# Kernel tuning notes

Hardware: AMD Instinct MI355X
Metric: run time of the kernel (lower is better)

The kernel has to match this reference:

```python
import math
import jax, jax.numpy as jnp
import numpy as np

B_, H_, L_, N_ = 64, 256, 1024, 64  # batch, n_feat, n_embd(=seq len), complex state modes (d_state=128 -> 64 conj pairs)


def setup_inputs() -> dict:
    key = jax.random.key(0)
    ks = jax.random.split(key, 12)
    x = jax.random.normal(ks[0], (B_, H_, L_), jnp.float32)
    t = jax.random.randint(ks[1], (B_,), 0, 1000)
    # AdaLayerNorm linear: n_embd -> 2*n_embd
    ada_w = jax.random.normal(ks[2], (2 * L_, L_), jnp.float32) * 0.02
    ada_b = jnp.zeros((2 * L_,), jnp.float32)
    # S4Layer prenorm (LayerNorm over n_feat, affine)
    norm_w = jnp.ones((H_,), jnp.float32)
    norm_b = jnp.zeros((H_,), jnp.float32)
    # S4D-style diagonal SSM parameters
    log_dt = math.log(0.001) + jax.random.uniform(ks[3], (H_,), jnp.float32) * (math.log(0.1) - math.log(0.001))
    A_re = jnp.full((H_, N_), math.log(0.5), jnp.float32)            # A_real = -exp(A_re) = -0.5
    A_im = jnp.ones((H_, 1), jnp.float32) * (math.pi * jnp.arange(N_, dtype=jnp.float32))[None, :]
    C_re = jax.random.normal(ks[4], (2, H_, N_), jnp.float32) * (N_ ** -0.5)  # 2 channels: bidirectional
    C_im = jax.random.normal(ks[5], (2, H_, N_), jnp.float32) * (N_ ** -0.5)
    D = jax.random.normal(ks[6], (H_,), jnp.float32)
    out_w = jax.random.normal(ks[7], (H_, H_), jnp.float32) * (H_ ** -0.5)   # S4 output 1x1 conv
    out_b = jnp.zeros((H_,), jnp.float32)
    lin1_w = jax.random.normal(ks[8], (H_, H_), jnp.float32) * (H_ ** -0.5)
    lin1_b = jnp.zeros((H_,), jnp.float32)
    lin2_w = jax.random.normal(ks[9], (H_, H_), jnp.float32) * (H_ ** -0.5)
    lin2_b = jnp.zeros((H_,), jnp.float32)
    return dict(x=x, t=t, ada_w=ada_w, ada_b=ada_b, norm_w=norm_w, norm_b=norm_b,
                log_dt=log_dt, A_re=A_re, A_im=A_im, C_re=C_re, C_im=C_im, D=D,
                out_w=out_w, out_b=out_b, lin1_w=lin1_w, lin1_b=lin1_b,
                lin2_w=lin2_w, lin2_b=lin2_b)


def _ln(v):
    m = v.mean(-1, keepdims=True)
    s = v.var(-1, keepdims=True)
    return (v - m) * jax.lax.rsqrt(s + 1e-5)


def _forward(t, x, ada_w, ada_b, norm_w, norm_b, log_dt, A_re, A_im, C_re, C_im, D,
             out_w, out_b, lin1_w, lin1_b, lin2_w, lin2_b):
    B, H, L = x.shape
    # ---- AdaLayerNorm over last dim (n_embd = L) ----
    half = L // 2
    freqs = jnp.exp(jnp.arange(half, dtype=jnp.float32) * (-math.log(10000.0) / (half - 1)))
    emb = t.astype(jnp.float32)[:, None] * freqs[None, :]
    emb = jnp.concatenate([jnp.sin(emb), jnp.cos(emb)], axis=-1)           # (B, L)
    emb = jax.nn.silu(emb) @ ada_w.T + ada_b                                # (B, 2L)
    scale, shift = jnp.split(emb[:, None, :], 2, axis=2)                    # (B,1,L)
    x = _ln(x) * (1.0 + scale) + shift                                      # (B,H,L)
    # ---- S4Layer: prenorm over channels ----
    z = (_ln(x.transpose(0, 2, 1)) * norm_w + norm_b).transpose(0, 2, 1)    # (B,H,L)
    # ---- S4 (diagonal SSM) bidirectional FFT convolution ----
    dt = jnp.exp(log_dt)                                                    # (H,)
    A = -jnp.exp(A_re) + 1j * A_im                                          # (H,N)
    dtA = dt[:, None] * A
    dA = jnp.exp(dtA)
    C = (C_re + 1j * C_im) * ((dA - 1.0) / A)                               # ZOH-discretized (2,H,N)
    vand = jnp.exp(dtA[:, :, None] * jnp.arange(L, dtype=jnp.float32))      # (H,N,L)
    K = 2.0 * jnp.real(jnp.einsum('chn,hnl->chl', C, vand))                 # (2,H,L)
    k = jnp.pad(K[0], ((0, 0), (0, L))) + jnp.pad(K[1][:, ::-1], ((0, 0), (L, 0)))  # (H,2L)
    n = 2 * L
    y = jnp.fft.irfft(jnp.fft.rfft(z, n=n) * jnp.fft.rfft(k, n=n), n=n)[..., :L]
    y = y + D[:, None] * z
    y = jax.nn.gelu(y, approximate=False)
    y = jnp.einsum('oi,bil->bol', out_w, y) + out_b[None, :, None]          # S4 output 1x1 conv
    x2 = y + x                                                              # residual
    # ---- gated output ----
    g = jnp.tanh(x2) * jax.nn.sigmoid(x2)
    out1 = jnp.einsum('oi,bil->bol', lin1_w, g) + lin1_b[None, :, None] + x
    out2 = jnp.einsum('oi,bil->bol', lin2_w, g) + lin2_b[None, :, None]
    return (out1, out2)


def reference(x, t, ada_w, ada_b, norm_w, norm_b, log_dt, A_re, A_im, C_re, C_im, D,
              out_w, out_b, lin1_w, lin1_b, lin2_w, lin2_b):
    return _forward(t, x, ada_w, ada_b, norm_w, norm_b, log_dt, A_re, A_im, C_re, C_im,
                    D, out_w, out_b, lin1_w, lin1_b, lin2_w, lin2_b)
```

## Files before the change

### kernel.cpp

```cpp
#include <hip/hip_runtime.h>
#include <math.h>

#define Bq 64
#define Hq 256
#define Lq 1024
#define HLq (Hq*Lq)
#define BHLq (Bq*Hq*Lq)
#define HNq (Hq*64)

typedef __attribute__((ext_vector_type(8))) short bf16x8;
typedef __attribute__((ext_vector_type(4))) float f32x4;

__device__ __forceinline__ float sigmoidf_(float x){ return 1.f/(1.f+expf(-x)); }
__device__ __forceinline__ unsigned short f2bf(float f){
  unsigned u = __float_as_uint(f);
  u += 0x7FFF + ((u>>16)&1);
  return (unsigned short)(u>>16);
}
__device__ __forceinline__ float bf2f(unsigned short h){ return __uint_as_float(((unsigned)h)<<16); }

__global__ __launch_bounds__(256) void k_ada2(const int* __restrict__ tptr,
        const float* __restrict__ ada_w, float* __restrict__ Part){
  __shared__ float Es[64][68];
  __shared__ float Ws[64][68];
  const int tid = threadIdx.x;
  const int o0 = blockIdx.x * 64;
  const int kc = blockIdx.y;
  const int k0 = kc * 64;
  const float ci = -logf(10000.f) / 511.f;
  #pragma unroll
  for (int it = 0; it < 4; ++it){
    int fidx = it*256 + tid;
    int row = fidx >> 4;
    int c4  = fidx & 15;
    float tb = (float)tptr[row];
    float4 v;
    float* vp = &v.x;
    #pragma unroll
    for (int q = 0; q < 4; ++q){
      int k = k0 + c4*4 + q;
      float f = expf(ci * (float)(k & 511));
      float arg = tb * f;
      float s = (k < 512) ? sinf(arg) : cosf(arg);
      vp[q] = s * sigmoidf_(s);
    }
    *(float4*)&Es[row][c4*4] = v;
  }
  #pragma unroll
  for (int it = 0; it < 4; ++it){
    int fidx = it*256 + tid;
    int row = fidx >> 4;
    int c4  = fidx & 15;
    *(float4*)&Ws[row][c4*4] = *(const float4*)(ada_w + (size_t)(o0+row)*1024 + k0 + c4*4);
  }
  __syncthreads();
  float acc[4][4] = {};
  #pragma unroll
  for (int ks = 0; ks < 16; ++ks){
    int k = ks*4;
    float4 ev[4], wv[4];
    #pragma unroll
    for (int i=0;i<4;++i) ev[i] = *(const float4*)&Es[(tid>>4) + 16*i][k];
    #pragma unroll
    for (int j=0;j<4;++j) wv[j] = *(const float4*)&Ws[(tid&15) + 16*j][k];
    #pragma unroll
    for (int i=0;i<4;++i)
      #pragma unroll
      for (int j=0;j<4;++j)
        acc[i][j] += ev[i].x*wv[j].x + ev[i].y*wv[j].y + ev[i].z*wv[j].z + ev[i].w*wv[j].w;
  }
  float* pbase = Part + (size_t)kc*131072 + o0;
  #pragma unroll
  for (int i=0;i<4;++i){
    int b = (tid>>4) + 16*i;
    #pragma unroll
    for (int j=0;j<4;++j){
      int o = (tid&15) + 16*j;
      pbase[(size_t)b*2048 + o] = acc[i][j];
    }
  }
}

__global__ void k_red(const float* __restrict__ Part, const float* __restrict__ ada_b,
                      float* __restrict__ scsh){
  int idx = blockIdx.x*256 + threadIdx.x;
  float4 s = ((const float4*)ada_b)[idx & 511];
  #pragma unroll
  for (int p = 0; p < 16; ++p){
    float4 u = ((const float4*)Part)[p*32768 + idx];
    s.x += u.x; s.y += u.y; s.z += u.z; s.w += u.w;
  }
  ((float4*)scsh)[idx] = s;
}

__global__ void k_wcvt(const float* __restrict__ w0, const float* __restrict__ w1,
                       const float* __restrict__ w2, unsigned short* __restrict__ wb){
  int idx = blockIdx.x*256 + threadIdx.x;
  const float* src = (idx < 16384) ? w0 : ((idx < 32768) ? w1 : w2);
  int loc = idx & 16383;
  float4 v = ((const float4*)src)[loc];
  uint2 pk;
  pk.x = (unsigned)f2bf(v.x) | ((unsigned)f2bf(v.y)<<16);
  pk.y = (unsigned)f2bf(v.z) | ((unsigned)f2bf(v.w)<<16);
  ((uint2*)wb)[idx] = pk;
}

__global__ void k_adaln(const float* __restrict__ x, const float* __restrict__ scsh,
                        float* __restrict__ A){
  const int bid = blockIdx.x;
  const int b = bid >> 8;
  const int tid = threadIdx.x;
  const float4* row = (const float4*)(x + (size_t)bid*1024);
  float4 v = row[tid];
  float s = v.x+v.y+v.z+v.w;
  float ss = v.x*v.x+v.y*v.y+v.z*v.z+v.w*v.w;
  #pragma unroll
  for (int off=32; off; off>>=1){ s += __shfl_xor(s,off); ss += __shfl_xor(ss,off); }
  __shared__ float rs_[4], rss_[4];
  int lane = tid & 63, w = tid >> 6;
  if (!lane){ rs_[w]=s; rss_[w]=ss; }
  __syncthreads();
  s  = rs_[0]+rs_[1]+rs_[2]+rs_[3];
  ss = rss_[0]+rss_[1]+rss_[2]+rss_[3];
  float mean = s * (1.f/1024.f);
  float var  = ss*(1.f/1024.f) - mean*mean;
  float rstd = rsqrtf(var + 1e-5f);
  float4 sc = ((const float4*)(scsh + b*2048))[tid];
  float4 sh = ((const float4*)(scsh + b*2048 + 1024))[tid];
  float4 o;
  o.x = (v.x-mean)*rstd*(1.f+sc.x) + sh.x;
  o.y = (v.y-mean)*rstd*(1.f+sc.y) + sh.y;
  o.z = (v.z-mean)*rstd*(1.f+sc.z) + sh.z;
  o.w = (v.w-mean)*rstd*(1.f+sc.w) + sh.w;
  ((float4*)(A + (size_t)bid*1024))[tid] = o;
}

__global__ void k_chln(const float* __restrict__ A, const float* __restrict__ nw,
                       const float* __restrict__ nb, unsigned short* __restrict__ Zb){
  const int b = blockIdx.y;
  const int l = blockIdx.x*256 + threadIdx.x;
  const float* base = A + (size_t)b*HLq + l;
  float s=0.f, ss=0.f;
  for (int h=0; h<256; ++h){ float v = base[h*1024]; s+=v; ss+=v*v; }
  float mean = s*(1.f/256.f);
  float var  = ss*(1.f/256.f) - mean*mean;
  float rstd = rsqrtf(var+1e-5f);
  unsigned short* zb = Zb + (size_t)b*HLq + l;
  for (int h=0; h<256; ++h){
    float v = base[h*1024];
    zb[h*1024] = f2bf((v-mean)*rstd*nw[h] + nb[h]);
  }
}

__global__ void k_ssmk(const float* __restrict__ log_dt, const float* __restrict__ A_re,
                       const float* __restrict__ A_im, const float* __restrict__ C_re,
                       const float* __restrict__ C_im, float* __restrict__ Kbuf){
  const int h = blockIdx.y;
  const int tid = threadIdx.x;
  __shared__ float dre[64], dim_[64], c0r[64], c0i[64], c1r[64], c1i[64];
  if (tid < 64){
    int n = tid;
    float dt = expf(log_dt[h]);
    float Ar = -expf(A_re[h*64+n]);
    float Ai = A_im[h*64+n];
    float dr = dt*Ar, di = dt*Ai;
    float er = expf(dr);
    float dAr = er*cosf(di), dAi = er*sinf(di);
    float den = Ar*Ar + Ai*Ai;
    float nr = dAr - 1.f, ni = dAi;
    float qr = (nr*Ar + ni*Ai)/den;
    float qi = (ni*Ar - nr*Ai)/den;
    float C0r = C_re[h*64+n],       C0i = C_im[h*64+n];
    float C1r = C_re[HNq + h*64+n], C1i = C_im[HNq + h*64+n];
    c0r[n] = C0r*qr - C0i*qi; c0i[n] = C0r*qi + C0i*qr;
    c1r[n] = C1r*qr - C1i*qi; c1i[n] = C1r*qi + C1i*qr;
    dre[n] = dr; dim_[n] = di;
  }
  __syncthreads();
  int l = blockIdx.x*256 + tid;
  float lf = (float)l;
  float a0=0.f, a1=0.f;
  for (int n=0;n<64;++n){
    float e  = expf(lf*dre[n]);
    float ph = lf*dim_[n];
    float wr = e*cosf(ph), wi = e*sinf(ph);
    a0 += c0r[n]*wr - c0i[n]*wi;
    a1 += c1r[n]*wr - c1i[n]*wi;
  }
  Kbuf[h*1024 + l]       = 2.f*a0;
  Kbuf[HLq + h*1024 + l] = 2.f*a1;
}

__global__ __launch_bounds__(256,2) void k_conv(const unsigned short* __restrict__ Zb,
        const float* __restrict__ Kbuf, const float* __restrict__ Dp,
        unsigned short* __restrict__ Cb){
  __shared__ unsigned short kcopy[8][2056];
  __shared__ unsigned short As[64][136];
  const int tid = threadIdx.x;
  const int h  = blockIdx.y;
  const int l0 = blockIdx.x * 512;
  const float* K0 = Kbuf + h*1024;
  const float* K1 = Kbuf + HLq + h*1024;
  for (int idx = tid; idx < 8*2056; idx += 256){
    int s = idx / 2056;
    int i = idx - s*2056;
    int q = 2046 - i - s;
    float v = 0.f;
    if (q >= 0) v = (q >= 1023) ? K0[q-1023] : K1[1022-q];
    kcopy[s][i] = f2bf(v);
  }
  const int lane = tid & 63;
  const int w    = tid >> 6;
  const int ln   = lane & 15;
  const int quad = lane >> 4;
  int kofs[8];
  #pragma unroll
  for (int nt=0; nt<8; ++nt){
    int l = l0 + w*128 + nt*16 + ln;
    int d = 1023 - l;
    int s = d & 7;
    kofs[nt] = s*2056 + (d - s) + quad*8;
  }
  const unsigned short* kbase = &kcopy[0][0];
  f32x4 acc[4][8] = {};
  for (int c = 0; c < 8; ++c){
    __syncthreads();
    #pragma unroll
    for (int pass = 0; pass < 4; ++pass){
      int b = pass*16 + (tid>>4);
      int col = (tid & 15)*8;
      *(uint4*)&As[b][col] = *(const uint4*)(Zb + ((size_t)b*256 + h)*1024 + c*128 + col);
    }
    __syncthreads();
    #pragma unroll
    for (int ks = 0; ks < 4; ++ks){
      int kk = ks*32 + quad*8;
      bf16x8 af[4];
      #pragma unroll
      for (int mt=0; mt<4; ++mt) af[mt] = *(const bf16x8*)&As[mt*16+ln][kk];
      int jb = c*128 + ks*32;
      bf16x8 bv[8];
      #pragma unroll
      for (int nt=0; nt<8; ++nt) bv[nt] = *(const bf16x8*)(kbase + kofs[nt] + jb);
      #pragma unroll
      for (int mt=0; mt<4; ++mt)
        #pragma unroll
        for (int nt=0; nt<8; ++nt)
          acc[mt][nt] = __builtin_amdgcn_mfma_f32_16x16x32_bf16(af[mt], bv[nt], acc[mt][nt], 0,0,0);
    }
  }
  float Dh = Dp[h];
  #pragma unroll
  for (int mt=0; mt<4; ++mt){
    #pragma unroll
    for (int reg=0; reg<4; ++reg){
      int b = mt*16 + quad*4 + reg;
      const unsigned short* zrow = Zb + ((size_t)b*256+h)*1024;
      unsigned short* crow = Cb + ((size_t)b*256+h)*1024;
      #pragma unroll
      for (int nt=0; nt<8; ++nt){
        int l = l0 + w*128 + nt*16 + ln;
        float y = acc[mt][nt][reg] + Dh*bf2f(zrow[l]);
        float g = 0.5f*y*(1.f + erff(y*0.70710678118f));
        crow[l] = f2bf(g);
      }
    }
  }
}

__global__ __launch_bounds__(512,2) void k_fuse(const unsigned short* __restrict__ U,
        const unsigned short* __restrict__ Wob, const float* __restrict__ out_b,
        const unsigned short* __restrict__ W1b, const float* __restrict__ b1,
        const unsigned short* __restrict__ W2b, const float* __restrict__ b2,
        const float* __restrict__ Ax, float* __restrict__ out){
  __shared__ unsigned short Us[64][280];
  __shared__ unsigned short Gs[64][280];
  const int tid = threadIdx.x;
  const int l0 = blockIdx.x * 64;
  const int b  = blockIdx.y;
  const int lane = tid & 63, w = tid >> 6, ln = lane & 15, quad = lane >> 4;
  {
    int l   = tid & 63;
    int grp = tid >> 6;
    #pragma unroll
    for (int it = 0; it < 8; ++it){
      int i4 = it*8 + grp;
      const unsigned short* usrc = U + ((size_t)b*256 + i4*4)*1024 + l0 + l;
      unsigned short e0 = usrc[0], e1 = usrc[1024], e2 = usrc[2048], e3 = usrc[3072];
      uint2 val; val.x = (unsigned)e0 | ((unsigned)e1<<16); val.y = (unsigned)e2 | ((unsigned)e3<<16);
      *(uint2*)&Us[l][i4*4] = val;
    }
  }
  __syncthreads();
  f32x4 acc[2][4] = {};
  #pragma unroll
  for (int ks = 0; ks < 8; ++ks){
    int kk = ks*32 + quad*8;
    bf16x8 af[2], bv[4];
    #pragma unroll
    for (int mt=0;mt<2;++mt) af[mt] = *(const bf16x8*)(Wob + (size_t)(w*32+mt*16+ln)*256 + kk);
    #pragma unroll
    for (int nt=0;nt<4;++nt) bv[nt] = *(const bf16x8*)&Us[nt*16+ln][kk];
    #pragma unroll
    for (int mt=0;mt<2;++mt)
      #pragma unroll
      for (int nt=0;nt<4;++nt)
        acc[mt][nt] = __builtin_amdgcn_mfma_f32_16x16x32_bf16(af[mt], bv[nt], acc[mt][nt],0,0,0);
  }
  float axv[2][4][4];
  #pragma unroll
  for (int mt=0;mt<2;++mt){
    #pragma unroll
    for (int reg=0;reg<4;++reg){
      int o = w*32 + mt*16 + quad*4 + reg;
      float bo = out_b[o];
      const float* arow = Ax + ((size_t)b*256 + o)*1024 + l0;
      #pragma unroll
      for (int nt=0;nt<4;++nt){
        int l = nt*16 + ln;
        float a = arow[l];
        axv[mt][nt][reg] = a;
        float v = acc[mt][nt][reg] + bo + a;
        acc[mt][nt][reg] = tanhf(v)*sigmoidf_(v);
      }
    }
  }
  #pragma unroll
  for (int mt=0;mt<2;++mt){
    int ob = w*32 + mt*16 + quad*4;
    #pragma unroll
    for (int nt=0;nt<4;++nt){
      uint2 pk;
      pk.x = (unsigned)f2bf(acc[mt][nt][0]) | ((unsigned)f2bf(acc[mt][nt][1])<<16);
      pk.y = (unsigned)f2bf(acc[mt][nt][2]) | ((unsigned)f2bf(acc[mt][nt][3])<<16);
      *(uint2*)&Gs[nt*16+ln][ob] = pk;
    }
  }
  __syncthreads();
  f32x4 acc1[2][4] = {}, acc2[2][4] = {};
  #pragma unroll
  for (int ks = 0; ks < 8; ++ks){
    int kk = ks*32 + quad*8;
    bf16x8 bv[4];
    #pragma unroll
    for (int nt=0;nt<4;++nt) bv[nt] = *(const bf16x8*)&Gs[nt*16+ln][kk];
    #pragma unroll
    for (int mt=0;mt<2;++mt){
      bf16x8 a1 = *(const bf16x8*)(W1b + (size_t)(w*32+mt*16+ln)*256 + kk);
      #pragma unroll
      for (int nt=0;nt<4;++nt)
        acc1[mt][nt] = __builtin_amdgcn_mfma_f32_16x16x32_bf16(a1, bv[nt], acc1[mt][nt],0,0,0);
      bf16x8 a2 = *(const bf16x8*)(W2b + (size_t)(w*32+mt*16+ln)*256 + kk);
      #pragma unroll
      for (int nt=0;nt<4;++nt)
        acc2[mt][nt] = __builtin_amdgcn_mfma_f32_16x16x32_bf16(a2, bv[nt], acc2[mt][nt],0,0,0);
    }
  }
  #pragma unroll
  for (int mt=0;mt<2;++mt){
    #pragma unroll
    for (int reg=0;reg<4;++reg){
      int o = w*32 + mt*16 + quad*4 + reg;
      float bo1 = b1[o], bo2 = b2[o];
      float* o1row = out + ((size_t)b*256 + o)*1024 + l0;
      float* o2row = o1row + BHLq;
      #pragma unroll
      for (int nt=0;nt<4;++nt){
        int l = nt*16 + ln;
        o1row[l] = acc1[mt][nt][reg] + bo1 + axv[mt][nt][reg];
        o2row[l] = acc2[mt][nt][reg] + bo2;
      }
    }
  }
}

extern "C" void kernel_launch(void* const* d_in, const int* in_sizes, int n_in,
                              void* d_out, int out_size, void* d_ws, size_t ws_size,
                              hipStream_t stream){
  const float* x      = (const float*)d_in[0];
  const int*   t      = (const int*)  d_in[1];
  const float* ada_w  = (const float*)d_in[2];
  const float* ada_b  = (const float*)d_in[3];
  const float* norm_w = (const float*)d_in[4];
  const float* norm_b = (const float*)d_in[5];
  const float* log_dt = (const float*)d_in[6];
  const float* A_re   = (const float*)d_in[7];
  const float* A_im   = (const float*)d_in[8];
  const float* C_re   = (const float*)d_in[9];
  const float* C_im   = (const float*)d_in[10];
  const float* Dp     = (const float*)d_in[11];
  const float* out_w  = (const float*)d_in[12];
  const float* out_b  = (const float*)d_in[13];
  const float* lin1_w = (const float*)d_in[14];
  const float* lin1_b = (const float*)d_in[15];
  const float* lin2_w = (const float*)d_in[16];
  const float* lin2_b = (const float*)d_in[17];

  float* Ax            = (float*)d_ws;
  unsigned short* Zb   = (unsigned short*)(Ax + BHLq);
  unsigned short* Cb   = Zb + BHLq;
  float* Kbuf          = (float*)(Cb + BHLq);
  float* Part          = Kbuf + 2*HLq;
  float* scsh          = Part + 16*64*2048;
  unsigned short* wb   = (unsigned short*)(scsh + 64*2048);
  float* out           = (float*)d_out;

  k_wcvt  <<<192, 256, 0, stream>>>(out_w, lin1_w, lin2_w, wb);
  k_ada2  <<<dim3(32, 16), 256, 0, stream>>>(t, ada_w, Part);
  k_red   <<<128, 256, 0, stream>>>(Part, ada_b, scsh);
  k_adaln <<<Bq*Hq, 256, 0, stream>>>(x, scsh, Ax);
  k_chln  <<<dim3(4, Bq), 256, 0, stream>>>(Ax, norm_w, norm_b, Zb);
  k_ssmk  <<<dim3(4, Hq), 256, 0, stream>>>(log_dt, A_re, A_im, C_re, C_im, Kbuf);
  k_conv  <<<dim3(2, Hq), 256, 0, stream>>>(Zb, Kbuf, Dp, Cb);
  k_fuse  <<<dim3(16, Bq), 512, 0, stream>>>(Cb, wb, out_b, wb + 65536, lin1_b,
                                             wb + 131072, lin2_b, Ax, out);
}
```

Before: 491.9 us.

## Raise k_fuse occupancy with a single swizzled LDS tile and split epilogue

The fused output-conv/gating/linear kernel now uses one XOR-swizzled LDS buffer for both the input tile and the gated tile, instead of two padded buffers. It no longer keeps the residual values in registers and splits the second GEMM into two halves, reading the residual again from global memory, to cut register pressure. Launch bounds request six blocks per CU instead of two. tanh*sigmoid is replaced by one exp-based algebraic form. In exchange the residual is read twice, an extra barrier is added, and register spills are possible under the tighter bound.

```diff
diff --git a/kernel.cpp b/kernel.cpp
--- a/kernel.cpp
+++ b/kernel.cpp
@@ -268,27 +268,27 @@
   }
 }
 
-__global__ __launch_bounds__(512,2) void k_fuse(const unsigned short* __restrict__ U,
+__global__ __launch_bounds__(512,6) void k_fuse(const unsigned short* __restrict__ U,
         const unsigned short* __restrict__ Wob, const float* __restrict__ out_b,
         const unsigned short* __restrict__ W1b, const float* __restrict__ b1,
         const unsigned short* __restrict__ W2b, const float* __restrict__ b2,
         const float* __restrict__ Ax, float* __restrict__ out){
-  __shared__ unsigned short Us[64][280];
-  __shared__ unsigned short Gs[64][280];
+  __shared__ unsigned short Ts[64][280];
   const int tid = threadIdx.x;
   const int l0 = blockIdx.x * 64;
   const int b  = blockIdx.y;
   const int lane = tid & 63, w = tid >> 6, ln = lane & 15, quad = lane >> 4;
   {
-    int l   = tid & 63;
-    int grp = tid >> 6;
+    int l = lane;
+    int s = (l >> 3) & 7;
     #pragma unroll
     for (int it = 0; it < 8; ++it){
-      int i4 = it*8 + grp;
+      int i4 = it*8 + w;
       const unsigned short* usrc = U + ((size_t)b*256 + i4*4)*1024 + l0 + l;
       unsigned short e0 = usrc[0], e1 = usrc[1024], e2 = usrc[2048], e3 = usrc[3072];
       uint2 val; val.x = (unsigned)e0 | ((unsigned)e1<<16); val.y = (unsigned)e2 | ((unsigned)e3<<16);
-      *(uint2*)&Us[l][i4*4] = val;
+      int p = i4 >> 1, hf = i4 & 1;
+      *(uint2*)&Ts[l][((p ^ s) << 3) + hf*4] = val;
     }
   }
   __syncthreads();
@@ -296,18 +296,22 @@
   #pragma unroll
   for (int ks = 0; ks < 8; ++ks){
     int kk = ks*32 + quad*8;
+    int p  = kk >> 3;
     bf16x8 af[2], bv[4];
     #pragma unroll
     for (int mt=0;mt<2;++mt) af[mt] = *(const bf16x8*)(Wob + (size_t)(w*32+mt*16+ln)*256 + kk);
     #pragma unroll
-    for (int nt=0;nt<4;++nt) bv[nt] = *(const bf16x8*)&Us[nt*16+ln][kk];
+    for (int nt=0;nt<4;++nt){
+      int l = nt*16 + ln;
+      int s = (l>>3) & 7;
+      bv[nt] = *(const bf16x8*)&Ts[l][(p ^ s) << 3];
+    }
     #pragma unroll
     for (int mt=0;mt<2;++mt)
       #pragma unroll
       for (int nt=0;nt<4;++nt)
         acc[mt][nt] = __builtin_amdgcn_mfma_f32_16x16x32_bf16(af[mt], bv[nt], acc[mt][nt],0,0,0);
   }
-  float axv[2][4][4];
   #pragma unroll
   for (int mt=0;mt<2;++mt){
     #pragma unroll
@@ -318,57 +322,69 @@
       #pragma unroll
       for (int nt=0;nt<4;++nt){
         int l = nt*16 + ln;
-        float a = arow[l];
-        axv[mt][nt][reg] = a;
-        float v = acc[mt][nt][reg] + bo + a;
-        acc[mt][nt][reg] = tanhf(v)*sigmoidf_(v);
+        float v = acc[mt][nt][reg] + bo + arow[l];
+        float t = expf(-fmaxf(v, -15.f));
+        acc[mt][nt][reg] = (1.f - t)/(1.f + t*t);
       }
     }
   }
+  __syncthreads();
   #pragma unroll
   for (int mt=0;mt<2;++mt){
-    int ob = w*32 + mt*16 + quad*4;
+    int i4 = w*8 + mt*4 + quad;
+    int p  = i4 >> 1, hf = i4 & 1;
     #pragma unroll
     for (int nt=0;nt<4;++nt){
+      int l = nt*16 + ln;
+      int s = (l>>3) & 7;
       uint2 pk;
       pk.x = (unsigned)f2bf(acc[mt][nt][0]) | ((unsigned)f2bf(acc[mt][nt][1])<<16);
       pk.y = (unsigned)f2bf(acc[mt][nt][2]) | ((unsigned)f2bf(acc[mt][nt][3])<<16);
-      *(uint2*)&Gs[nt*16+ln][ob] = pk;
-    }
-  }
-  __syncthreads();
-  f32x4 acc1[2][4] = {}, acc2[2][4] = {};
-  #pragma unroll
-  for (int ks = 0; ks < 8; ++ks){
-    int kk = ks*32 + quad*8;
-    bf16x8 bv[4];
-    #pragma unroll
-    for (int nt=0;nt<4;++nt) bv[nt] = *(const bf16x8*)&Gs[nt*16+ln][kk];
+      *(uint2*)&Ts[l][((p ^ s) << 3) + hf*4] = pk;
+    }
+  }
+  __syncthreads();
+  #pragma unroll
+  for (int half = 0; half < 2; ++half){
+    f32x4 acc1[2][2] = {}, acc2[2][2] = {};
+    #pragma unroll
+    for (int ks = 0; ks < 8; ++ks){
+      int kk = ks*32 + quad*8;
+      int p  = kk >> 3;
+      bf16x8 bv[2];
+      #pragma unroll
+      for (int nt=0;nt<2;++nt){
+        int l = (half*2 + nt)*16 + ln;
+        int s = (l>>3) & 7;
+        bv[nt] = *(const bf16x8*)&Ts[l][(p ^ s) << 3];
+      }
+      #pragma unroll
+      for (int mt=0;mt<2;++mt){
+        bf16x8 a1 = *(const bf16x8*)(W1b + (size_t)(w*32+mt*16+ln)*256 + kk);
+        #pragma unroll
+        for (int nt=0;nt<2;++nt)
+          acc1[mt][nt] = __builtin_amdgcn_mfma_f32_16x16x32_bf16(a1, bv[nt], acc1[mt][nt],0,0,0);
+        bf16x8 a2 = *(const bf16x8*)(W2b + (size_t)(w*32+mt*16+ln)*256 + kk);
+        #pragma unroll
+        for (int nt=0;nt<2;++nt)
+          acc2[mt][nt] = __builtin_amdgcn_mfma_f32_16x16x32_bf16(a2, bv[nt], acc2[mt][nt],0,0,0);
+      }
+    }
     #pragma unroll
     for (int mt=0;mt<2;++mt){
-      bf16x8 a1 = *(const bf16x8*)(W1b + (size_t)(w*32+mt*16+ln)*256 + kk);
-      #pragma unroll
-      for (int nt=0;nt<4;++nt)
-        acc1[mt][nt] = __builtin_amdgcn_mfma_f32_16x16x32_bf16(a1, bv[nt], acc1[mt][nt],0,0,0);
-      bf16x8 a2 = *(const bf16x8*)(W2b + (size_t)(w*32+mt*16+ln)*256 + kk);
-      #pragma unroll
-      for (int nt=0;nt<4;++nt)
-        acc2[mt][nt] = __builtin_amdgcn_mfma_f32_16x16x32_bf16(a2, bv[nt], acc2[mt][nt],0,0,0);
-    }
-  }
-  #pragma unroll
-  for (int mt=0;mt<2;++mt){
-    #pragma unroll
-    for (int reg=0;reg<4;++reg){
-      int o = w*32 + mt*16 + quad*4 + reg;
-      float bo1 = b1[o], bo2 = b2[o];
-      float* o1row = out + ((size_t)b*256 + o)*1024 + l0;
-      float* o2row = o1row + BHLq;
-      #pragma unroll
-      for (int nt=0;nt<4;++nt){
-        int l = nt*16 + ln;
-        o1row[l] = acc1[mt][nt][reg] + bo1 + axv[mt][nt][reg];
-        o2row[l] = acc2[mt][nt][reg] + bo2;
+      #pragma unroll
+      for (int reg=0;reg<4;++reg){
+        int o = w*32 + mt*16 + quad*4 + reg;
+        float bo1 = b1[o], bo2 = b2[o];
+        const float* arow = Ax + ((size_t)b*256 + o)*1024 + l0;
+        float* o1row = out + ((size_t)b*256 + o)*1024 + l0;
+        float* o2row = o1row + BHLq;
+        #pragma unroll
+        for (int nt=0;nt<2;++nt){
+          int l = (half*2 + nt)*16 + ln;
+          o1row[l] = acc1[mt][nt][reg] + bo1 + arow[l];
+          o2row[l] = acc2[mt][nt][reg] + bo2;
+        }
       }
     }
   }
```

Result: slower. 620.9 us (+26.2%).

## Parallelize channel LayerNorm over feature chunks and slim fused GEMM kernel resources

Applied to the files above, without the earlier changes.

The channel LayerNorm kernel is restructured so four warps each reduce a quarter of the 256 features and combine partial sums through shared memory, launching four times as many blocks to raise parallelism on a memory-bound pass. The fused output kernel reuses a single shared tile for both the input and gated activations, drops the cached residual registers, computes the second GEMM in two halves to cut live accumulators, and raises the launch-bounds occupancy target to 3. tanh*sigmoid is rewritten as a single exp, (1-t)/(1+t^2) with clamping, which cuts transcendental calls. The cost is re-reading the residual from global memory and an extra barrier.

```diff
diff --git a/kernel.cpp b/kernel.cpp
--- a/kernel.cpp
+++ b/kernel.cpp
@@ -135,20 +135,37 @@
   ((float4*)(A + (size_t)bid*1024))[tid] = o;
 }
 
-__global__ void k_chln(const float* __restrict__ A, const float* __restrict__ nw,
-                       const float* __restrict__ nb, unsigned short* __restrict__ Zb){
-  const int b = blockIdx.y;
-  const int l = blockIdx.x*256 + threadIdx.x;
-  const float* base = A + (size_t)b*HLq + l;
-  float s=0.f, ss=0.f;
-  for (int h=0; h<256; ++h){ float v = base[h*1024]; s+=v; ss+=v*v; }
-  float mean = s*(1.f/256.f);
-  float var  = ss*(1.f/256.f) - mean*mean;
-  float rstd = rsqrtf(var+1e-5f);
+__global__ __launch_bounds__(256) void k_chln2(const float* __restrict__ A,
+        const float* __restrict__ nw, const float* __restrict__ nb,
+        unsigned short* __restrict__ Zb){
+  const int b  = blockIdx.y;
+  const int lt = threadIdx.x & 63;
+  const int hc = threadIdx.x >> 6;
+  const int l  = blockIdx.x*64 + lt;
+  const float* p = A + (size_t)b*HLq + (size_t)hc*64*1024 + l;
+  float s = 0.f, ss = 0.f;
+  #pragma unroll 8
+  for (int h = 0; h < 64; ++h){ float v = p[(size_t)h*1024]; s += v; ss += v*v; }
+  __shared__ float sp[4][64], ssp[4][64];
+  __shared__ float mS[64], rS[64];
+  sp[hc][lt] = s; ssp[hc][lt] = ss;
+  __syncthreads();
+  if (threadIdx.x < 64){
+    int li = threadIdx.x;
+    float st  = sp[0][li]+sp[1][li]+sp[2][li]+sp[3][li];
+    float sst = ssp[0][li]+ssp[1][li]+ssp[2][li]+ssp[3][li];
+    float m = st*(1.f/256.f);
+    float var = sst*(1.f/256.f) - m*m;
+    mS[li] = m; rS[li] = rsqrtf(var + 1e-5f);
+  }
+  __syncthreads();
+  float m = mS[lt], r = rS[lt];
   unsigned short* zb = Zb + (size_t)b*HLq + l;
-  for (int h=0; h<256; ++h){
-    float v = base[h*1024];
-    zb[h*1024] = f2bf((v-mean)*rstd*nw[h] + nb[h]);
+  #pragma unroll 4
+  for (int h = 0; h < 64; ++h){
+    int hh = hc*64 + h;
+    float v = p[(size_t)h*1024];
+    zb[(size_t)hh*1024] = f2bf((v-m)*r*nw[hh] + nb[hh]);
   }
 }
 
@@ -268,13 +285,13 @@
   }
 }
 
-__global__ __launch_bounds__(512,2) void k_fuse(const unsigned short* __restrict__ U,
+__global__ __launch_bounds__(512,3)
+void k_fuse(const unsigned short* __restrict__ U,
         const unsigned short* __restrict__ Wob, const float* __restrict__ out_b,
         const unsigned short* __restrict__ W1b, const float* __restrict__ b1,
         const unsigned short* __restrict__ W2b, const float* __restrict__ b2,
         const float* __restrict__ Ax, float* __restrict__ out){
-  __shared__ unsigned short Us[64][280];
-  __shared__ unsigned short Gs[64][280];
+  __shared__ unsigned short Ts[64][264];
   const int tid = threadIdx.x;
   const int l0 = blockIdx.x * 64;
   const int b  = blockIdx.y;
@@ -288,11 +305,11 @@
       const unsigned short* usrc = U + ((size_t)b*256 + i4*4)*1024 + l0 + l;
       unsigned short e0 = usrc[0], e1 = usrc[1024], e2 = usrc[2048], e3 = usrc[3072];
       uint2 val; val.x = (unsigned)e0 | ((unsigned)e1<<16); val.y = (unsigned)e2 | ((unsigned)e3<<16);
-      *(uint2*)&Us[l][i4*4] = val;
-    }
-  }
-  __syncthreads();
-  f32x4 acc[2][4] = {};
+      *(uint2*)&Ts[l][i4*4] = val;
+    }
+  }
+  __syncthreads();
+  f32x4 acc1[2][4] = {};
   #pragma unroll
   for (int ks = 0; ks < 8; ++ks){
     int kk = ks*32 + quad*8;
@@ -300,14 +317,13 @@
     #pragma unroll
     for (int mt=0;mt<2;++mt) af[mt] = *(const bf16x8*)(Wob + (size_t)(w*32+mt*16+ln)*256 + kk);
     #pragma unroll
-    for (int nt=0;nt<4;++nt) bv[nt] = *(const bf16x8*)&Us[nt*16+ln][kk];
+    for (int nt=0;nt<4;++nt) bv[nt] = *(const bf16x8*)&Ts[nt*16+ln][kk];
     #pragma unroll
     for (int mt=0;mt<2;++mt)
       #pragma unroll
       for (int nt=0;nt<4;++nt)
-        acc[mt][nt] = __builtin_amdgcn_mfma_f32_16x16x32_bf16(af[mt], bv[nt], acc[mt][nt],0,0,0);
-  }
-  float axv[2][4][4];
+        acc1[mt][nt] = __builtin_amdgcn_mfma_f32_16x16x32_bf16(af[mt], bv[nt], acc1[mt][nt],0,0,0);
+  }
   #pragma unroll
   for (int mt=0;mt<2;++mt){
     #pragma unroll
@@ -318,57 +334,57 @@
       #pragma unroll
       for (int nt=0;nt<4;++nt){
         int l = nt*16 + ln;
-        float a = arow[l];
-        axv[mt][nt][reg] = a;
-        float v = acc[mt][nt][reg] + bo + a;
-        acc[mt][nt][reg] = tanhf(v)*sigmoidf_(v);
+        float v = acc1[mt][nt][reg] + bo + arow[l];
+        float t = expf(-fmaxf(v, -15.f));
+        acc1[mt][nt][reg] = (1.f - t)/(1.f + t*t);
       }
     }
   }
+  __syncthreads();
   #pragma unroll
   for (int mt=0;mt<2;++mt){
     int ob = w*32 + mt*16 + quad*4;
     #pragma unroll
     for (int nt=0;nt<4;++nt){
+      int l = nt*16 + ln;
       uint2 pk;
-      pk.x = (unsigned)f2bf(acc[mt][nt][0]) | ((unsigned)f2bf(acc[mt][nt][1])<<16);
-      pk.y = (unsigned)f2bf(acc[mt][nt][2]) | ((unsigned)f2bf(acc[mt][nt][3])<<16);
-      *(uint2*)&Gs[nt*16+ln][ob] = pk;
-    }
-  }
-  __syncthreads();
-  f32x4 acc1[2][4] = {}, acc2[2][4] = {};
-  #pragma unroll
-  for (int ks = 0; ks < 8; ++ks){
-    int kk = ks*32 + quad*8;
-    bf16x8 bv[4];
-    #pragma unroll
-    for (int nt=0;nt<4;++nt) bv[nt] = *(const bf16x8*)&Gs[nt*16+ln][kk];
-    #pragma unroll
-    for (int mt=0;mt<2;++mt){
-      bf16x8 a1 = *(const bf16x8*)(W1b + (size_t)(w*32+mt*16+ln)*256 + kk);
+      pk.x = (unsigned)f2bf(acc1[mt][nt][0]) | ((unsigned)f2bf(acc1[mt][nt][1])<<16);
+      pk.y = (unsigned)f2bf(acc1[mt][nt][2]) | ((unsigned)f2bf(acc1[mt][nt][3])<<16);
+      *(uint2*)&Ts[l][ob] = pk;
+    }
+  }
+  __syncthreads();
+  #pragma unroll
+  for (int half = 0; half < 2; ++half){
+    f32x4 accA[4] = {}, accB[4] = {};
+    #pragma unroll
+    for (int ks = 0; ks < 8; ++ks){
+      int kk = ks*32 + quad*8;
+      bf16x8 bv[4];
+      #pragma unroll
+      for (int nt=0;nt<4;++nt) bv[nt] = *(const bf16x8*)&Ts[nt*16+ln][kk];
+      int orow = w*32 + half*16 + ln;
+      bf16x8 a1 = *(const bf16x8*)(W1b + (size_t)orow*256 + kk);
       #pragma unroll
       for (int nt=0;nt<4;++nt)
-        acc1[mt][nt] = __builtin_amdgcn_mfma_f32_16x16x32_bf16(a1, bv[nt], acc1[mt][nt],0,0,0);
-      bf16x8 a2 = *(const bf16x8*)(W2b + (size_t)(w*32+mt*16+ln)*256 + kk);
+        accA[nt] = __builtin_amdgcn_mfma_f32_16x16x32_bf16(a1, bv[nt], accA[nt],0,0,0);
+      bf16x8 a2 = *(const bf16x8*)(W2b + (size_t)orow*256 + kk);
       #pragma unroll
       for (int nt=0;nt<4;++nt)
-        acc2[mt][nt] = __builtin_amdgcn_mfma_f32_16x16x32_bf16(a2, bv[nt], acc2[mt][nt],0,0,0);
-    }
-  }
-  #pragma unroll
-  for (int mt=0;mt<2;++mt){
+        accB[nt] = __builtin_amdgcn_mfma_f32_16x16x32_bf16(a2, bv[nt], accB[nt],0,0,0);
+    }
     #pragma unroll
     for (int reg=0;reg<4;++reg){
-      int o = w*32 + mt*16 + quad*4 + reg;
+      int o = w*32 + half*16 + quad*4 + reg;
       float bo1 = b1[o], bo2 = b2[o];
+      const float* arow = Ax + ((size_t)b*256 + o)*1024 + l0;
       float* o1row = out + ((size_t)b*256 + o)*1024 + l0;
       float* o2row = o1row + BHLq;
       #pragma unroll
       for (int nt=0;nt<4;++nt){
         int l = nt*16 + ln;
-        o1row[l] = acc1[mt][nt][reg] + bo1 + axv[mt][nt][reg];
-        o2row[l] = acc2[mt][nt][reg] + bo2;
+        o1row[l] = accA[nt][reg] + bo1 + arow[l];
+        o2row[l] = accB[nt][reg] + bo2;
       }
     }
   }
@@ -409,7 +425,7 @@
   k_ada2  <<<dim3(32, 16), 256, 0, stream>>>(t, ada_w, Part);
   k_red   <<<128, 256, 0, stream>>>(Part, ada_b, scsh);
   k_adaln <<<Bq*Hq, 256, 0, stream>>>(x, scsh, Ax);
-  k_chln  <<<dim3(4, Bq), 256, 0, stream>>>(Ax, norm_w, norm_b, Zb);
+  k_chln2 <<<dim3(16, Bq), 256, 0, stream>>>(Ax, norm_w, norm_b, Zb);
   k_ssmk  <<<dim3(4, Hq), 256, 0, stream>>>(log_dt, A_re, A_im, C_re, C_im, Kbuf);
   k_conv  <<<dim3(2, Hq), 256, 0, stream>>>(Zb, Kbuf, Dp, Cb);
   k_fuse  <<<dim3(16, Bq), 512, 0, stream>>>(Cb, wb, out_b, wb + 65536, lin1_b,
```

After: 453.2 us. -7.9%, faster.
